# Optimization experiments

Hardware: AMD Instinct MI355X
Metric: run time of the kernel (lower is better)

Reference implementation:

```python
import jax, jax.numpy as jnp
import numpy as np
from jax import lax

B, C, N = 8, 3, 65536
NUM_POINTS = 1024


def setup_inputs() -> dict:
    key = jax.random.key(0)
    points = jax.random.normal(key, (B, C, N), dtype=jnp.float32)
    return {"points": points}


def furthest_point_sampling(xyz, num_points):
    # xyz: (B, N, 3) -> indices (B, num_points), int32
    b, n, _ = xyz.shape
    init_idx = jnp.zeros((b,), dtype=jnp.int32)  # CUDA FPS seeds with index 0
    init_dists = jnp.full((b, n), 1e10, dtype=xyz.dtype)

    def step(carry, _):
        dists, last_idx = carry
        last_pt = jnp.take_along_axis(xyz, last_idx[:, None, None], axis=1)  # (B,1,3)
        d = jnp.sum(jnp.square(xyz - last_pt), axis=-1)  # (B,N) squared dist to newest pt
        dists = jnp.minimum(dists, d)
        nxt = jnp.argmax(dists, axis=-1).astype(jnp.int32)
        return (dists, nxt), nxt

    (_, _), rest = lax.scan(step, (init_dists, init_idx), None, length=num_points - 1)
    # rest: (num_points-1, B) -> (B, num_points)
    idx = jnp.concatenate([init_idx[None, :], rest], axis=0).T
    return idx


def reference(points):
    # points: (B, 3, N), channels-first as in the torch module
    xyz = jnp.transpose(points, (0, 2, 1))  # (B, N, 3)
    idx = furthest_point_sampling(xyz, NUM_POINTS)  # (B, num_points)
    # fps_gather_by_index: gather along point axis of (B, 3, N)
    new_points = jnp.take_along_axis(points, idx[:, None, :], axis=2)  # (B, 3, num_points)
    return new_points
```

## Files before the change

kernel.cpp:

```cpp
#include <hip/hip_runtime.h>


namespace {

constexpr int kB = 8;
constexpr int kN = 65536;
constexpr int kNP = 1024;
constexpr int kPB = 16;
constexpr int kThreads = 256;
constexpr int kPPT = kN / (kPB * kThreads);
constexpr int kGrp = kPPT / 4;
constexpr int kWaves = kThreads / 64;
constexpr int kRgn = 16;

__device__ __forceinline__ unsigned long long u64max(unsigned long long a,
                                                     unsigned long long b) {
  return a > b ? a : b;
}

template <int CTRL>
__device__ __forceinline__ unsigned long long dpp_u64_zero(unsigned long long v) {
  const unsigned lo =
      (unsigned)__builtin_amdgcn_update_dpp(0, (int)(unsigned)v, CTRL, 0xf, 0xf, false);
  const unsigned hi =
      (unsigned)__builtin_amdgcn_update_dpp(0, (int)(unsigned)(v >> 32), CTRL, 0xf, 0xf, false);
  return ((unsigned long long)hi << 32) | lo;
}

__device__ __forceinline__ unsigned long long wave_max_u64(unsigned long long v) {
  v = u64max(v, dpp_u64_zero<0x111>(v));
  v = u64max(v, dpp_u64_zero<0x112>(v));
  v = u64max(v, dpp_u64_zero<0x114>(v));
  v = u64max(v, dpp_u64_zero<0x118>(v));
  v = u64max(v, dpp_u64_zero<0x142>(v));
  v = u64max(v, dpp_u64_zero<0x143>(v));
  const unsigned lo = (unsigned)__builtin_amdgcn_readlane((int)(unsigned)v, 63);
  const unsigned hi = (unsigned)__builtin_amdgcn_readlane((int)(unsigned)(v >> 32), 63);
  return ((unsigned long long)hi << 32) | lo;
}

__global__ __launch_bounds__(kThreads) void fps_kernel(const float* __restrict__ pts,
                                                       float* __restrict__ out,
                                                       unsigned long long* __restrict__ slots) {
  const int batch = blockIdx.x & 7;
  const int slice = blockIdx.x >> 3;
  const int tid = threadIdx.x;
  const int lane = tid & 63;
  const int wave = tid >> 6;

  const float* __restrict__ xb = pts + (size_t)batch * 3 * kN;
  const float* __restrict__ yb = xb + kN;
  const float* __restrict__ zb = xb + 2 * kN;

  __shared__ unsigned long long s_wkey[kWaves];
  __shared__ float s_q[3];
  __shared__ unsigned s_win[2];
  __shared__ int s_hist[kNP];

  if (tid == 0) {
    s_win[0] = 0xFFFFFFFFu;
    s_win[1] = 0xFFFFFFFFu;
  }

  const int sbase = slice * (kThreads * kPPT);
  const int base0 = sbase + tid * 4;
  float px[kPPT], py[kPPT], pz[kPPT], dist[kPPT];
#pragma unroll
  for (int g = 0; g < kGrp; ++g) {
    const int base = base0 + g * (kThreads * 4);
    const float4 vx = *reinterpret_cast<const float4*>(xb + base);
    const float4 vy = *reinterpret_cast<const float4*>(yb + base);
    const float4 vz = *reinterpret_cast<const float4*>(zb + base);
    px[g * 4 + 0] = vx.x; px[g * 4 + 1] = vx.y; px[g * 4 + 2] = vx.z; px[g * 4 + 3] = vx.w;
    py[g * 4 + 0] = vy.x; py[g * 4 + 1] = vy.y; py[g * 4 + 2] = vy.z; py[g * 4 + 3] = vy.w;
    pz[g * 4 + 0] = vz.x; pz[g * 4 + 1] = vz.y; pz[g * 4 + 2] = vz.z; pz[g * 4 + 3] = vz.w;
  }
#pragma unroll
  for (int k = 0; k < kPPT; ++k) dist[k] = 1e10f;

  float qx = xb[0], qy = yb[0], qz = zb[0];

  unsigned long long* const sb = slots + (size_t)batch * kRgn * kPB;

  for (int it = 1; it < kNP; ++it) {
    const unsigned tag = (unsigned)it;

    float bd = -1.0f;
    int bi = 0;
#pragma unroll
    for (int g = 0; g < kGrp; ++g) {
#pragma unroll
      for (int j = 0; j < 4; ++j) {
        const int k = g * 4 + j;
        const float dx = px[k] - qx;
        const float dy = py[k] - qy;
        const float dz = pz[k] - qz;
        const float ss =
            __fadd_rn(__fadd_rn(__fmul_rn(dx, dx), __fmul_rn(dy, dy)), __fmul_rn(dz, dz));
        const float nd = fminf(dist[k], ss);
        dist[k] = nd;
        if (nd > bd) {
          bd = nd;
          bi = base0 + g * (kThreads * 4) + j;
        }
      }
    }

    unsigned long long key = ((unsigned long long)__float_as_uint(bd) << 32) |
                             ((unsigned long long)(0xFFFFu - (unsigned)bi) << 16) |
                             (unsigned long long)tag;

    key = wave_max_u64(key);
    if (lane == 0) s_wkey[wave] = key;
    __syncthreads();

    if (wave == 0) {
      unsigned long long bk = s_wkey[lane & (kWaves - 1)];
      bk = wave_max_u64(bk);

      unsigned long long* const rgn = sb + (size_t)(it & (kRgn - 1)) * kPB;
      if (lane == 0) {
        __hip_atomic_store(rgn + slice, bk, __ATOMIC_RELAXED, __HIP_MEMORY_SCOPE_AGENT);
      }

      const unsigned long long* const myslot = rgn + (lane & (kPB - 1));
      float cx = 0.f, cy = 0.f, cz = 0.f;
      bool have = false;
      unsigned long long w;
      unsigned long long a =
          __hip_atomic_load(myslot, __ATOMIC_RELAXED, __HIP_MEMORY_SCOPE_AGENT);
      for (;;) {
        unsigned long long b =
            __hip_atomic_load(myslot, __ATOMIC_RELAXED, __HIP_MEMORY_SCOPE_AGENT);
        const bool va = (unsigned)(a & 0xFFFFull) == tag;
        if ((lane < kPB) && va && !have) {
          const int ci = (int)(0xFFFFu - ((unsigned)(a >> 16) & 0xFFFFu));
          cx = xb[ci];
          cy = yb[ci];
          cz = zb[ci];
          have = true;
        }
        if (__all(va)) {
          w = a;
          break;
        }
        a = b;
      }

      const unsigned long long mx = wave_max_u64(w);
      const int wi = (int)(0xFFFFu - ((unsigned)(mx >> 16) & 0xFFFFu));
      const int winslot = wi >> 12;
      qx = __shfl(cx, winslot, 64);
      qy = __shfl(cy, winslot, 64);
      qz = __shfl(cz, winslot, 64);
      if (lane == 0) {
        s_hist[it] = wi;
        s_q[0] = qx;
        s_q[1] = qy;
        s_q[2] = qz;
        __hip_atomic_store(&s_win[it & 1], ((unsigned)wi << 16) | tag, __ATOMIC_RELEASE,
                           __HIP_MEMORY_SCOPE_WORKGROUP);
      }
    } else {
      unsigned v;
      do {
        v = __hip_atomic_load(&s_win[it & 1], __ATOMIC_ACQUIRE, __HIP_MEMORY_SCOPE_WORKGROUP);
      } while ((v & 0xFFFFu) != tag);
      qx = s_q[0];
      qy = s_q[1];
      qz = s_q[2];
    }
  }

  __syncthreads();

  if (slice == 0) {
    float* __restrict__ ob = out + (size_t)batch * 3 * kNP;
    for (int j = tid; j < kNP; j += kThreads) {
      const int id = (j == 0) ? 0 : s_hist[j];
      ob[j] = xb[id];
      ob[kNP + j] = yb[id];
      ob[2 * kNP + j] = zb[id];
    }
  }
}

}

extern "C" void kernel_launch(void* const* d_in, const int* in_sizes, int n_in,
                              void* d_out, int out_size, void* d_ws, size_t ws_size,
                              hipStream_t stream) {
  (void)in_sizes;
  (void)n_in;
  (void)out_size;
  (void)ws_size;
  const float* pts = (const float*)d_in[0];
  float* out = (float*)d_out;
  unsigned long long* slots = (unsigned long long*)d_ws;
  fps_kernel<<<dim3(kB * kPB), dim3(kThreads), 0, stream>>>(pts, out, slots);
}
```

Measured before the change: 1.729 ms.

## Add dedicated poller wave and replace per-iteration barrier with LDS counter

Adds a fifth wave to each block whose only job is to poll the cross-block global slots and publish the winning point to shared memory. The four scan waves no longer hit a __syncthreads each iteration. Each one bumps a shared atomic counter, and the last to arrive combines the four wave keys and stores the block result to global memory. The aim is to take the block-wide barrier and the wave-0 double duty off the critical path of each serial FPS step. The cost is an extra wave that spins on global memory and LDS atomic contention.

```diff
diff --git a/kernel.cpp b/kernel.cpp
--- a/kernel.cpp
+++ b/kernel.cpp
@@ -7,10 +7,11 @@
 constexpr int kN = 65536;
 constexpr int kNP = 1024;
 constexpr int kPB = 16;
-constexpr int kThreads = 256;
-constexpr int kPPT = kN / (kPB * kThreads);
+constexpr int kScanWaves = 4;
+constexpr int kScanThreads = kScanWaves * 64;
+constexpr int kThreads = kScanThreads + 64;
+constexpr int kPPT = kN / (kPB * kScanThreads);
 constexpr int kGrp = kPPT / 4;
-constexpr int kWaves = kThreads / 64;
 constexpr int kRgn = 16;
 
 __device__ __forceinline__ unsigned long long u64max(unsigned long long a,
@@ -52,85 +53,102 @@
   const float* __restrict__ yb = xb + kN;
   const float* __restrict__ zb = xb + 2 * kN;
 
-  __shared__ unsigned long long s_wkey[kWaves];
+  __shared__ unsigned long long s_wkey[kScanWaves];
+  __shared__ unsigned s_cnt;
   __shared__ float s_q[3];
   __shared__ unsigned s_win[2];
   __shared__ int s_hist[kNP];
 
   if (tid == 0) {
+    s_cnt = 0;
     s_win[0] = 0xFFFFFFFFu;
     s_win[1] = 0xFFFFFFFFu;
   }
-
-  const int sbase = slice * (kThreads * kPPT);
-  const int base0 = sbase + tid * 4;
-  float px[kPPT], py[kPPT], pz[kPPT], dist[kPPT];
-#pragma unroll
-  for (int g = 0; g < kGrp; ++g) {
-    const int base = base0 + g * (kThreads * 4);
-    const float4 vx = *reinterpret_cast<const float4*>(xb + base);
-    const float4 vy = *reinterpret_cast<const float4*>(yb + base);
-    const float4 vz = *reinterpret_cast<const float4*>(zb + base);
-    px[g * 4 + 0] = vx.x; px[g * 4 + 1] = vx.y; px[g * 4 + 2] = vx.z; px[g * 4 + 3] = vx.w;
-    py[g * 4 + 0] = vy.x; py[g * 4 + 1] = vy.y; py[g * 4 + 2] = vy.z; py[g * 4 + 3] = vy.w;
-    pz[g * 4 + 0] = vz.x; pz[g * 4 + 1] = vz.y; pz[g * 4 + 2] = vz.z; pz[g * 4 + 3] = vz.w;
-  }
-#pragma unroll
-  for (int k = 0; k < kPPT; ++k) dist[k] = 1e10f;
-
-  float qx = xb[0], qy = yb[0], qz = zb[0];
+  __syncthreads();
 
   unsigned long long* const sb = slots + (size_t)batch * kRgn * kPB;
 
-  for (int it = 1; it < kNP; ++it) {
-    const unsigned tag = (unsigned)it;
-
-    float bd = -1.0f;
-    int bi = 0;
+  if (wave < kScanWaves) {
+    const int sbase = slice * (kScanThreads * kPPT);
+    const int base0 = sbase + tid * 4;
+    float px[kPPT], py[kPPT], pz[kPPT], dist[kPPT];
 #pragma unroll
     for (int g = 0; g < kGrp; ++g) {
-#pragma unroll
-      for (int j = 0; j < 4; ++j) {
-        const int k = g * 4 + j;
-        const float dx = px[k] - qx;
-        const float dy = py[k] - qy;
-        const float dz = pz[k] - qz;
-        const float ss =
-            __fadd_rn(__fadd_rn(__fmul_rn(dx, dx), __fmul_rn(dy, dy)), __fmul_rn(dz, dz));
-        const float nd = fminf(dist[k], ss);
-        dist[k] = nd;
-        if (nd > bd) {
-          bd = nd;
-          bi = base0 + g * (kThreads * 4) + j;
-        }
-      }
-    }
-
-    unsigned long long key = ((unsigned long long)__float_as_uint(bd) << 32) |
-                             ((unsigned long long)(0xFFFFu - (unsigned)bi) << 16) |
-                             (unsigned long long)tag;
-
-    key = wave_max_u64(key);
-    if (lane == 0) s_wkey[wave] = key;
-    __syncthreads();
-
-    if (wave == 0) {
-      unsigned long long bk = s_wkey[lane & (kWaves - 1)];
-      bk = wave_max_u64(bk);
-
-      unsigned long long* const rgn = sb + (size_t)(it & (kRgn - 1)) * kPB;
+      const int base = base0 + g * (kScanThreads * 4);
+      const float4 vx = *reinterpret_cast<const float4*>(xb + base);
+      const float4 vy = *reinterpret_cast<const float4*>(yb + base);
+      const float4 vz = *reinterpret_cast<const float4*>(zb + base);
+      px[g * 4 + 0] = vx.x; px[g * 4 + 1] = vx.y; px[g * 4 + 2] = vx.z; px[g * 4 + 3] = vx.w;
+      py[g * 4 + 0] = vy.x; py[g * 4 + 1] = vy.y; py[g * 4 + 2] = vy.z; py[g * 4 + 3] = vy.w;
+      pz[g * 4 + 0] = vz.x; pz[g * 4 + 1] = vz.y; pz[g * 4 + 2] = vz.z; pz[g * 4 + 3] = vz.w;
+    }
+#pragma unroll
+    for (int k = 0; k < kPPT; ++k) dist[k] = 1e10f;
+
+    float qx = xb[0], qy = yb[0], qz = zb[0];
+
+    for (int it = 1; it < kNP; ++it) {
+      const unsigned tag = (unsigned)it;
+
+      float bd = -1.0f;
+      int bi = 0;
+#pragma unroll
+      for (int g = 0; g < kGrp; ++g) {
+#pragma unroll
+        for (int j = 0; j < 4; ++j) {
+          const int k = g * 4 + j;
+          const float dx = px[k] - qx;
+          const float dy = py[k] - qy;
+          const float dz = pz[k] - qz;
+          const float ss =
+              __fadd_rn(__fadd_rn(__fmul_rn(dx, dx), __fmul_rn(dy, dy)), __fmul_rn(dz, dz));
+          const float nd = fminf(dist[k], ss);
+          dist[k] = nd;
+          if (nd > bd) {
+            bd = nd;
+            bi = base0 + g * (kScanThreads * 4) + j;
+          }
+        }
+      }
+
+      unsigned long long key = ((unsigned long long)__float_as_uint(bd) << 32) |
+                               ((unsigned long long)(0xFFFFu - (unsigned)bi) << 16) |
+                               (unsigned long long)tag;
+
+      key = wave_max_u64(key);
       if (lane == 0) {
-        __hip_atomic_store(rgn + slice, bk, __ATOMIC_RELAXED, __HIP_MEMORY_SCOPE_AGENT);
-      }
-
-      const unsigned long long* const myslot = rgn + (lane & (kPB - 1));
+        s_wkey[wave] = key;
+        const unsigned n =
+            __hip_atomic_fetch_add(&s_cnt, 1u, __ATOMIC_ACQ_REL, __HIP_MEMORY_SCOPE_WORKGROUP);
+        if (n == 4u * (unsigned)it - 1u) {
+          unsigned long long bk = s_wkey[0];
+          bk = u64max(bk, s_wkey[1]);
+          bk = u64max(bk, s_wkey[2]);
+          bk = u64max(bk, s_wkey[3]);
+          __hip_atomic_store(sb + (size_t)(it & (kRgn - 1)) * kPB + slice, bk,
+                             __ATOMIC_RELAXED, __HIP_MEMORY_SCOPE_AGENT);
+        }
+      }
+
+      unsigned v;
+      do {
+        v = __hip_atomic_load(&s_win[it & 1], __ATOMIC_ACQUIRE, __HIP_MEMORY_SCOPE_WORKGROUP);
+      } while ((v & 0xFFFFu) != tag);
+      qx = s_q[0];
+      qy = s_q[1];
+      qz = s_q[2];
+    }
+  } else {
+    for (int it = 1; it < kNP; ++it) {
+      const unsigned tag = (unsigned)it;
+      const unsigned long long* const myslot =
+          sb + (size_t)(it & (kRgn - 1)) * kPB + (lane & (kPB - 1));
+
       float cx = 0.f, cy = 0.f, cz = 0.f;
       bool have = false;
       unsigned long long w;
-      unsigned long long a =
-          __hip_atomic_load(myslot, __ATOMIC_RELAXED, __HIP_MEMORY_SCOPE_AGENT);
       for (;;) {
-        unsigned long long b =
+        const unsigned long long a =
             __hip_atomic_load(myslot, __ATOMIC_RELAXED, __HIP_MEMORY_SCOPE_AGENT);
         const bool va = (unsigned)(a & 0xFFFFull) == tag;
         if ((lane < kPB) && va && !have) {
@@ -144,15 +162,14 @@
           w = a;
           break;
         }
-        a = b;
       }
 
       const unsigned long long mx = wave_max_u64(w);
       const int wi = (int)(0xFFFFu - ((unsigned)(mx >> 16) & 0xFFFFu));
       const int winslot = wi >> 12;
-      qx = __shfl(cx, winslot, 64);
-      qy = __shfl(cy, winslot, 64);
-      qz = __shfl(cz, winslot, 64);
+      const float qx = __shfl(cx, winslot, 64);
+      const float qy = __shfl(cy, winslot, 64);
+      const float qz = __shfl(cz, winslot, 64);
       if (lane == 0) {
         s_hist[it] = wi;
         s_q[0] = qx;
@@ -161,14 +178,6 @@
         __hip_atomic_store(&s_win[it & 1], ((unsigned)wi << 16) | tag, __ATOMIC_RELEASE,
                            __HIP_MEMORY_SCOPE_WORKGROUP);
       }
-    } else {
-      unsigned v;
-      do {
-        v = __hip_atomic_load(&s_win[it & 1], __ATOMIC_ACQUIRE, __HIP_MEMORY_SCOPE_WORKGROUP);
-      } while ((v & 0xFFFFu) != tag);
-      qx = s_q[0];
-      qy = s_q[1];
-      qz = s_q[2];
     }
   }
 
```

Result: slower. 2.588 ms (+49.7%).
